# Kernel optimization log

Measured on AMD Instinct MI355X. Metric: run time of the kernel, lower is better.

## Reference

```python
import jax, jax.numpy as jnp
import numpy as np

B, T, C, NH = 2, 2048, 1024, 16
HD = C // NH  # 64


def _ln(x, g, b, eps=1e-5):
    m = x.mean(-1, keepdims=True)
    v = ((x - m) ** 2).mean(-1, keepdims=True)
    return (x - m) / jnp.sqrt(v + eps) * g + b


def _ff(x, w1, b1, w2, b2):
    # Linear -> exact (erf) GELU -> Linear; dropout=0 (identity)
    return jax.nn.gelu(x @ w1 + b1, approximate=False) @ w2 + b2


def setup_inputs() -> dict:
    key = jax.random.key(0)
    ks = jax.random.split(key, 16)
    s = 0.02
    f32 = jnp.float32
    return {
        "x": jax.random.normal(ks[0], (B, T, C), f32),
        # SelfAttn qkv projection (torch Linear stored transposed: (in, out))
        "w_attn": jax.random.normal(ks[1], (C, 3 * C), f32) * s,
        "b_attn": jnp.zeros((3 * C,), f32),
        # SelfAttn's internal FeedForward
        "wa1": jax.random.normal(ks[2], (C, 4 * C), f32) * s,
        "ba1": jnp.zeros((4 * C,), f32),
        "wa2": jax.random.normal(ks[3], (4 * C, C), f32) * s,
        "ba2": jnp.zeros((C,), f32),
        # Block ln1
        "g1": jnp.ones((C,), f32),
        "be1": jnp.zeros((C,), f32),
        # Block FeedForward
        "wf1": jax.random.normal(ks[4], (C, 4 * C), f32) * s,
        "bf1": jnp.zeros((4 * C,), f32),
        "wf2": jax.random.normal(ks[5], (4 * C, C), f32) * s,
        "bf2": jnp.zeros((C,), f32),
        # Block ln2
        "g2": jnp.ones((C,), f32),
        "be2": jnp.zeros((C,), f32),
    }


def reference(x, w_attn, b_attn, wa1, ba1, wa2, ba2, g1, be1,
              wf1, bf1, wf2, bf2, g2, be2):
    Bx, Tx, Cx = x.shape
    qkv = x @ w_attn + b_attn  # (B, T, 3C)
    # NOTE: original splits as K, Q, V (in that order)
    K, Q, V = jnp.split(qkv, 3, axis=-1)

    def heads(t):  # (B, T, C) -> (B, NH, T, HD)
        return t.reshape(Bx, Tx, NH, HD).transpose(0, 2, 1, 3)

    Q, K, V = heads(Q), heads(K), heads(V)
    att = jnp.einsum('bhqd,bhkd->bhqk', Q, K) / np.float32(np.sqrt(HD))
    mask = jnp.tril(jnp.ones((Tx, Tx), bool))  # causal
    att = jnp.where(mask, att, -jnp.inf)
    att = jax.nn.softmax(att, axis=-1)
    y = jnp.einsum('bhqk,bhkd->bhqd', att, V)
    y = y.transpose(0, 2, 1, 3).reshape(Bx, Tx, Cx)
    # SelfAttn applies its own FeedForward (no output projection)
    y = _ff(y, wa1, ba1, wa2, ba2)
    # Block: post-sublayer LayerNorm, additive residuals
    x = x + _ln(y, g1, be1)
    x = x + _ln(_ff(x, wf1, bf1, wf2, bf2), g2, be2)
    return x
```

## Files before the change

### kernel.cpp

```cpp
#include <hip/hip_runtime.h>
#include <hip/hip_bf16.h>
#include <math.h>

#define Bz 2
#define Tz 2048
#define Cz 1024
#define NHz 16
#define HDz 64
#define Mz (Bz*Tz)

typedef unsigned short u16;
typedef __attribute__((ext_vector_type(8))) short bf16x8;
typedef __attribute__((ext_vector_type(4))) float f32x4;

__device__ __forceinline__ float bf2f(u16 u){
  union { unsigned int i; float f; } v; v.i = ((unsigned int)u) << 16; return v.f;
}
__device__ __forceinline__ u16 f2bf(float f){
  union { float f; unsigned int i; } v; v.f = f;
  return (u16)((v.i + 0x7fffu + ((v.i >> 16) & 1u)) >> 16);
}
__device__ __forceinline__ unsigned pack_bf_trunc(float a, float b){
  union { float f; unsigned u; } ua, ub; ua.f = a; ub.f = b;
  return (ua.u >> 16) | (ub.u & 0xffff0000u);
}
__device__ __forceinline__ float gelu_fast(float x){
  float x3 = x * x * x;
  float z2 = 1.5957691216057308f * (x + 0.044715f * x3);
  float e  = __expf(z2);
  float t  = 1.f - 2.f / (e + 1.f);
  return 0.5f * x * (1.f + t);
}

__device__ __forceinline__ void glds16(const void* g, void* l){
  __builtin_amdgcn_global_load_lds(
      (const __attribute__((address_space(1))) void*)g,
      (__attribute__((address_space(3))) void*)l, 16, 0, 0);
}

__device__ __forceinline__ void pbar(){
  asm volatile("" ::: "memory");
  __builtin_amdgcn_s_barrier();
  asm volatile("" ::: "memory");
}
#define VMCNT(n) asm volatile("s_waitcnt vmcnt(" #n ")" ::: "memory")

__global__ __launch_bounds__(256) void prep_kernel(
    const float* __restrict__ xin, u16* __restrict__ xout,
    const float* __restrict__ s0, const float* __restrict__ s1,
    const float* __restrict__ s2, const float* __restrict__ s3,
    const float* __restrict__ s4,
    u16* __restrict__ d0, u16* __restrict__ d1, u16* __restrict__ d2,
    u16* __restrict__ d3, u16* __restrict__ d4){
  if (blockIdx.x < 4096) {
    int i = blockIdx.x * 256 + threadIdx.x;
    float4 v = ((const float4*)xin)[i];
    u16 t[4] = { f2bf(v.x), f2bf(v.y), f2bf(v.z), f2bf(v.w) };
    *(uint2*)&xout[(size_t)i * 4] = *(const uint2*)t;
    return;
  }
  __shared__ float tile[32][33];
  const int t = blockIdx.x - 4096;
  const float* src; u16* dst; int K, N, local;
  if (t < 3072)       { src = s0; dst = d0; K = 1024; N = 3072; local = t; }
  else if (t < 7168)  { src = s1; dst = d1; K = 1024; N = 4096; local = t - 3072; }
  else if (t < 11264) { src = s2; dst = d2; K = 4096; N = 1024; local = t - 7168; }
  else if (t < 15360) { src = s3; dst = d3; K = 1024; N = 4096; local = t - 11264; }
  else                { src = s4; dst = d4; K = 4096; N = 1024; local = t - 15360; }
  const int NT = N >> 5;
  const int kb = (local / NT) * 32, nb = (local % NT) * 32;
  const int tx = threadIdx.x & 31, ty = threadIdx.x >> 5;
  #pragma unroll
  for (int r = ty; r < 32; r += 8)
    tile[r][tx] = src[(size_t)(kb + r) * N + nb + tx];
  __syncthreads();
  #pragma unroll
  for (int r = ty; r < 32; r += 8)
    dst[(size_t)(nb + r) * K + kb + tx] = f2bf(tile[tx][r]);
}

template<int ACT, int KLEN>
__global__ __launch_bounds__(512, 2) void gemm256_kernel(const u16* __restrict__ A,
                                                         const u16* __restrict__ Bt,
                                                         const float* __restrict__ bias,
                                                         u16* __restrict__ ob,
                                                         int N, int lda){
  __shared__ __align__(16) u16 As[2][256 * 64];
  __shared__ __align__(16) u16 Bs[2][256 * 64];
  const int tid  = threadIdx.x;
  const int lane = tid & 63;
  const int wave = tid >> 6;
  const int cc = lane & 15, quad = lane >> 4;
  const int wm = (wave >> 2) * 128;
  const int wn = (wave & 3) * 64;

  int flat = blockIdx.x + gridDim.x * blockIdx.y;
  const int nwg = gridDim.x * gridDim.y;
  flat = (flat & 7) * (nwg >> 3) + (flat >> 3);
  const int m0 = (flat & 15) * 256;
  const int n0 = (flat >> 4) * 256;

  const u16* Ak  = A  + (size_t)blockIdx.z * KLEN;
  const u16* Btk = Bt + (size_t)blockIdx.z * KLEN;

  int srow[2], scol[2];
  #pragma unroll
  for (int rnd = 0; rnd < 2; ++rnd) {
    const int ci = tid + rnd * 512;
    const int r = ci >> 3, cg = ci & 7;
    srow[rnd] = r;
    scol[rnd] = (cg ^ (r & 7)) * 8;
  }
  int colsw[2];
  #pragma unroll
  for (int s = 0; s < 2; ++s)
    colsw[s] = (s * 32 + quad * 8) ^ ((cc & 7) << 3);

  const auto stA = [&](int t) {
    u16* dstb = As[t & 1];
    const u16* src = Ak + (size_t)m0 * lda + t * 64;
    #pragma unroll
    for (int h = 0; h < 2; ++h)
      #pragma unroll
      for (int rnd = 0; rnd < 2; ++rnd)
        glds16(src + (size_t)(h * 128 + srow[rnd]) * lda + scol[rnd],
               dstb + h * 8192 + (tid + rnd * 512) * 8);
  };
  const auto stB = [&](int t) {
    u16* dstb = Bs[t & 1];
    const u16* src = Btk + (size_t)n0 * lda + t * 64;
    #pragma unroll
    for (int h = 0; h < 2; ++h)
      #pragma unroll
      for (int rnd = 0; rnd < 2; ++rnd)
        glds16(src + (size_t)(h * 128 + srow[rnd]) * lda + scol[rnd],
               dstb + h * 8192 + (tid + rnd * 512) * 8);
  };

  bf16x8 af[4][2];
  bf16x8 bfr[2][2][2];
  f32x4 acc[2][2][4][2] = {};

  const auto rdA = [&](int qa, int bsel) {
    #pragma unroll
    for (int f = 0; f < 4; ++f)
      #pragma unroll
      for (int s = 0; s < 2; ++s)
        af[f][s] = *(const bf16x8*)&As[bsel][(wm + qa * 64 + f * 16 + cc) * 64 + colsw[s]];
  };
  const auto rdB = [&](int qb, int bsel) {
    #pragma unroll
    for (int f = 0; f < 2; ++f)
      #pragma unroll
      for (int s = 0; s < 2; ++s)
        bfr[qb][f][s] = *(const bf16x8*)&Bs[bsel][(wn + qb * 32 + f * 16 + cc) * 64 + colsw[s]];
  };
  const auto mf32 = [&](int qa) {
    __builtin_amdgcn_s_setprio(1);
    #pragma unroll
    for (int qb = 0; qb < 2; ++qb)
      #pragma unroll
      for (int s = 0; s < 2; ++s)
        #pragma unroll
        for (int am = 0; am < 4; ++am)
          #pragma unroll
          for (int bn = 0; bn < 2; ++bn)
            acc[qa][qb][am][bn] = __builtin_amdgcn_mfma_f32_16x16x32_bf16(
                af[am][s], bfr[qb][bn][s], acc[qa][qb][am][bn], 0, 0, 0);
    __builtin_amdgcn_s_setprio(0);
  };
  const auto mf32b = [&](int qa) {
    __builtin_amdgcn_s_setprio(1);
    #pragma unroll
    for (int qb = 1; qb >= 0; --qb)
      #pragma unroll
      for (int s = 0; s < 2; ++s)
        #pragma unroll
        for (int am = 0; am < 4; ++am)
          #pragma unroll
          for (int bn = 0; bn < 2; ++bn)
            acc[qa][qb][am][bn] = __builtin_amdgcn_mfma_f32_16x16x32_bf16(
                af[am][s], bfr[qb][bn][s], acc[qa][qb][am][bn], 0, 0, 0);
    __builtin_amdgcn_s_setprio(0);
  };

  stB(0); stA(0);
  stB(1);
  VMCNT(4);
  pbar();

  constexpr int nIter = KLEN >> 7;
  for (int i = 0; i < nIter; ++i) {
    const int t = 2 * i;
    const bool more = (i + 1 < nIter);
    rdA(0, 0); rdB(0, 0); rdB(1, 0); stA(t + 1);
    pbar(); mf32(0); pbar();
    rdA(1, 0); if (more) stB(t + 2);
    pbar(); mf32b(1);
    if (more) { VMCNT(4); } else { VMCNT(0); }
    pbar();
    rdA(0, 1); rdB(0, 1); rdB(1, 1); if (more) stA(t + 2);
    pbar(); mf32(0); pbar();
    rdA(1, 1); if (more) stB(t + 3);
    pbar(); mf32b(1);
    if (more) { VMCNT(4); }
    pbar();
  }

  u16* obz = ob + (size_t)blockIdx.z * ((size_t)Mz * N);
  const float* bp = (blockIdx.z == 0) ? bias : nullptr;
  const int rbase = quad * 4;
  #pragma unroll
  for (int qa = 0; qa < 2; ++qa)
    #pragma unroll
    for (int qb = 0; qb < 2; ++qb)
      #pragma unroll
      for (int bn = 0; bn < 2; ++bn) {
        const int col = n0 + wn + qb * 32 + bn * 16 + cc;
        const float bv = bp ? bp[col] : 0.f;
        #pragma unroll
        for (int am = 0; am < 4; ++am)
          #pragma unroll
          for (int r = 0; r < 4; ++r) {
            const int row = m0 + wm + qa * 64 + am * 16 + rbase + r;
            float v = acc[qa][qb][am][bn][r] + bv;
            if (ACT == 1) v = gelu_fast(v);
            obz[(size_t)row * N + col] = f2bf(v);
          }
      }
}

__global__ __launch_bounds__(256) void vtrans_kernel(const u16* __restrict__ qkv,
                                                     u16* __restrict__ Vtb){
  __shared__ u16 Vl[64 * 72];
  const int tid = threadIdx.x;
  const int t0 = blockIdx.x * 64, h = blockIdx.y, b = blockIdx.z;
  const int bh = b * NHz + h;
  #pragma unroll
  for (int it = 0; it < 2; it++) {
    int c = tid + it * 256;
    int row = c >> 3, g = c & 7;
    *(uint4*)&Vl[row * 72 + g * 8] =
        *(const uint4*)(qkv + (size_t)(b * Tz + t0 + row) * (3 * Cz) + 2 * Cz + h * 64 + g * 8);
  }
  __syncthreads();
  #pragma unroll
  for (int it = 0; it < 2; it++) {
    int c = tid + it * 256;
    int d = c >> 3, tg = c & 7;
    u16 tmp[8];
    #pragma unroll
    for (int e = 0; e < 8; e++) tmp[e] = Vl[(tg * 8 + e) * 72 + d];
    *(uint4*)&Vtb[((size_t)bh * 64 + d) * Tz + t0 + tg * 8] = *(const uint4*)tmp;
  }
}

__global__ __launch_bounds__(256) void attn_kernel(const u16* __restrict__ qkv,
                                                   const u16* __restrict__ Vtb,
                                                   u16* __restrict__ y){
  __shared__ __align__(16) u16 KV[2][2][64 * 64];
  __shared__ __align__(16) u16 Ps[64 * 72];
  const int tid = threadIdx.x;
  const int lane = tid & 63, wave = tid >> 6;
  const int cc = lane & 15, quad = lane >> 4;
  const int flat = blockIdx.x;
  const int xcd = flat & 7, slot = flat >> 3;
  const int bhg = xcd * 4 + (slot >> 4);
  const int qtp = slot & 15;
  const int h = bhg & 15, b = bhg >> 4;
  const int bh = b * NHz + h;
  const size_t rowb = (size_t)b * Tz;
  const int wq0 = wave * 16;

  int foff[4][2];
  const int sw0 = (quad ^ (cc & 7)) * 8;
  const int sw1 = ((4 + quad) ^ (cc & 7)) * 8;
  #pragma unroll
  for (int t = 0; t < 4; ++t) {
    foff[t][0] = (t * 16 + cc) * 64 + sw0;
    foff[t][1] = (t * 16 + cc) * 64 + sw1;
  }
  const int pswb = (wq0 + cc) * 72 + quad * 4;
  const int psr0 = (wq0 + cc) * 72 + quad * 8;
  const int psr1 = (wq0 + cc) * 72 + 32 + quad * 8;

  auto stage = [&](int i, int bsel) {
    const int k0s = i * 64;
    #pragma unroll
    for (int it = 0; it < 2; ++it) {
      int ci = tid + it * 256;
      int row = ci >> 3, g = ci & 7;
      int gs = g ^ (row & 7);
      glds16(qkv + (rowb + k0s + row) * (3 * Cz) + h * 64 + gs * 8, &KV[bsel][0][ci * 8]);
      glds16(Vtb + ((size_t)bh * 64 + row) * Tz + k0s + gs * 8,     &KV[bsel][1][ci * 8]);
    }
  };

  for (int ph = 0; ph < 2; ++ph) {
    const int qt = ph ? (31 - qtp) : qtp;
    const int q0t = qt * 64 + wq0;
    const int nkt = qt + 1;
    const int wqmax = q0t + 15;

    bf16x8 qf[2];
    #pragma unroll
    for (int s = 0; s < 2; ++s)
      qf[s] = *(const bf16x8*)(qkv + (rowb + q0t + cc) * (3 * Cz)
                               + Cz + h * 64 + s * 32 + quad * 8);
    f32x4 acc[4] = {};
    float lp = 0.f;

    if (ph) __syncthreads();
    stage(0, 0);

    for (int i = 0; i < nkt; ++i) {
      __syncthreads();
      if (i + 1 < nkt) stage(i + 1, (i + 1) & 1);
      const int sel = i & 1;
      const u16* Kl = KV[sel][0];
      const u16* Vl = KV[sel][1];
      const int k0 = i * 64;
      if (k0 > wqmax) continue;

      bf16x8 kf[4][2];
      #pragma unroll
      for (int kt = 0; kt < 4; ++kt) {
        kf[kt][0] = *(const bf16x8*)&Kl[foff[kt][0]];
        kf[kt][1] = *(const bf16x8*)&Kl[foff[kt][1]];
      }
      const int qbase = q0t;
      #pragma unroll
      for (int kt = 0; kt < 4; ++kt) {
        const int kbase = k0 + kt * 16;
        uint2 pk;
        if (kbase > qbase + 15) {
          pk.x = 0u; pk.y = 0u;
        } else {
          f32x4 st = __builtin_amdgcn_mfma_f32_16x16x32_bf16(
              kf[kt][0], qf[0], (f32x4){0.f, 0.f, 0.f, 0.f}, 0, 0, 0);
          st = __builtin_amdgcn_mfma_f32_16x16x32_bf16(kf[kt][1], qf[1], st, 0, 0, 0);
          if (kbase + 15 > qbase) {
            const int kq = kbase + quad * 4, ql = qbase + cc;
            st[0] = (kq     <= ql) ? st[0] : -1e30f;
            st[1] = (kq + 1 <= ql) ? st[1] : -1e30f;
            st[2] = (kq + 2 <= ql) ? st[2] : -1e30f;
            st[3] = (kq + 3 <= ql) ? st[3] : -1e30f;
          }
          float p0 = __expf(fmaf(st[0], 0.125f, -16.f));
          float p1 = __expf(fmaf(st[1], 0.125f, -16.f));
          float p2 = __expf(fmaf(st[2], 0.125f, -16.f));
          float p3 = __expf(fmaf(st[3], 0.125f, -16.f));
          lp += (p0 + p1) + (p2 + p3);
          pk.x = pack_bf_trunc(p0, p1);
          pk.y = pack_bf_trunc(p2, p3);
        }
        *(uint2*)&Ps[pswb + kt * 16] = pk;
      }
      bf16x8 pf0 = *(const bf16x8*)&Ps[psr0];
      bf16x8 pf1 = *(const bf16x8*)&Ps[psr1];
      #pragma unroll
      for (int jd = 0; jd < 4; ++jd) {
        bf16x8 vf0 = *(const bf16x8*)&Vl[foff[jd][0]];
        bf16x8 vf1 = *(const bf16x8*)&Vl[foff[jd][1]];
        acc[jd] = __builtin_amdgcn_mfma_f32_16x16x32_bf16(pf0, vf0, acc[jd], 0, 0, 0);
        acc[jd] = __builtin_amdgcn_mfma_f32_16x16x32_bf16(pf1, vf1, acc[jd], 0, 0, 0);
      }
    }

    lp += __shfl_xor(lp, 16, 64);
    lp += __shfl_xor(lp, 32, 64);
    float inv[4];
    #pragma unroll
    for (int r = 0; r < 4; ++r) inv[r] = 1.f / __shfl(lp, quad * 4 + r, 64);
    #pragma unroll
    for (int jd = 0; jd < 4; ++jd)
      #pragma unroll
      for (int r = 0; r < 4; ++r) {
        int qrow = q0t + quad * 4 + r;
        y[(rowb + qrow) * Cz + h * 64 + jd * 16 + cc] = f2bf(acc[jd][r] * inv[r]);
      }
  }
}

__global__ __launch_bounds__(256) void ln_resid_kernel(const float* __restrict__ xf,
                                                       const u16* __restrict__ xb16,
                                                       const u16* __restrict__ yp,
                                                       const float* __restrict__ g,
                                                       const float* __restrict__ be,
                                                       float* __restrict__ outf,
                                                       u16* __restrict__ outb){
  const int row = blockIdx.x;
  const int c0 = threadIdx.x * 4;
  const size_t base = (size_t)row * Cz + c0;
  float4 v; v.x = 0.f; v.y = 0.f; v.z = 0.f; v.w = 0.f;
  #pragma unroll
  for (int p = 0; p < 4; ++p) {
    uint2 pp = *(const uint2*)(yp + (size_t)p * ((size_t)Mz * Cz) + base);
    v.x += bf2f((u16)(pp.x & 0xffff)); v.y += bf2f((u16)(pp.x >> 16));
    v.z += bf2f((u16)(pp.y & 0xffff)); v.w += bf2f((u16)(pp.y >> 16));
  }
  float s  = v.x + v.y + v.z + v.w;
  float s2 = v.x*v.x + v.y*v.y + v.z*v.z + v.w*v.w;
  #pragma unroll
  for (int off = 32; off > 0; off >>= 1) {
    s  += __shfl_down(s,  off);
    s2 += __shfl_down(s2, off);
  }
  __shared__ float ps[4], ps2[4];
  int wave = threadIdx.x >> 6, lane = threadIdx.x & 63;
  if (lane == 0) { ps[wave] = s; ps2[wave] = s2; }
  __syncthreads();
  s  = ps[0]  + ps[1]  + ps[2]  + ps[3];
  s2 = ps2[0] + ps2[1] + ps2[2] + ps2[3];
  const float mean = s * (1.f / Cz);
  const float var  = s2 * (1.f / Cz) - mean * mean;
  const float rstd = rsqrtf(var + 1e-5f);
  float4 xv;
  if (xf) {
    xv = *(const float4*)(xf + base);
  } else {
    uint2 px = *(const uint2*)(xb16 + base);
    xv.x = bf2f((u16)(px.x & 0xffff)); xv.y = bf2f((u16)(px.x >> 16));
    xv.z = bf2f((u16)(px.y & 0xffff)); xv.w = bf2f((u16)(px.y >> 16));
  }
  float4 gv = *(const float4*)(g + c0);
  float4 bv = *(const float4*)(be + c0);
  float4 ov;
  ov.x = xv.x + (v.x - mean) * rstd * gv.x + bv.x;
  ov.y = xv.y + (v.y - mean) * rstd * gv.y + bv.y;
  ov.z = xv.z + (v.z - mean) * rstd * gv.z + bv.z;
  ov.w = xv.w + (v.w - mean) * rstd * gv.w + bv.w;
  if (outf) *(float4*)(outf + base) = ov;
  if (outb) {
    u16 t[4] = { f2bf(ov.x), f2bf(ov.y), f2bf(ov.z), f2bf(ov.w) };
    *(ulonglong1*)&outb[base] = *(const ulonglong1*)t;
  }
}

extern "C" void kernel_launch(void* const* d_in, const int* in_sizes, int n_in,
                              void* d_out, int out_size, void* d_ws, size_t ws_size,
                              hipStream_t stream) {
  const float* x      = (const float*)d_in[0];
  const float* w_attn = (const float*)d_in[1];
  const float* b_attn = (const float*)d_in[2];
  const float* wa1    = (const float*)d_in[3];
  const float* ba1    = (const float*)d_in[4];
  const float* wa2    = (const float*)d_in[5];
  const float* ba2    = (const float*)d_in[6];
  const float* g1     = (const float*)d_in[7];
  const float* be1    = (const float*)d_in[8];
  const float* wf1    = (const float*)d_in[9];
  const float* bf1    = (const float*)d_in[10];
  const float* wf2    = (const float*)d_in[11];
  const float* bf2    = (const float*)d_in[12];
  const float* g2     = (const float*)d_in[13];
  const float* be2    = (const float*)d_in[14];
  float* out = (float*)d_out;

  char* ws = (char*)d_ws;
  size_t off = 0;
  auto alloc = [&](size_t bytes) { size_t o = off; off += (bytes + 255) & ~(size_t)255; return o; };
  u16* qkvb    = (u16*)(ws + alloc((size_t)Mz * 3 * Cz * 2));
  u16* ybuf    = (u16*)(ws + alloc((size_t)Mz * Cz * 2));
  u16* xb      = (u16*)(ws + alloc((size_t)Mz * Cz * 2));
  u16* wT_attn = (u16*)(ws + alloc((size_t)3 * Cz * Cz * 2));
  u16* wT_a1   = (u16*)(ws + alloc((size_t)4 * Cz * Cz * 2));
  u16* Vtb     = (u16*)(ws + alloc((size_t)Bz * NHz * HDz * Tz * 2));
  u16* wT_a2   = (u16*)(ws + alloc((size_t)4 * Cz * Cz * 2));
  u16* wT_f1   = (u16*)(ws + alloc((size_t)4 * Cz * Cz * 2));
  u16* wT_f2   = (u16*)(ws + alloc((size_t)4 * Cz * Cz * 2));
  u16* hbuf    = (u16*)(ws + alloc((size_t)Mz * 4 * Cz * 2));
  u16* pb      = (u16*)(ws + alloc((size_t)4 * Mz * Cz * 2));
  u16* x1b     = (u16*)(ws + alloc((size_t)Mz * Cz * 2));
  alloc(256);
  (void)ws_size; (void)in_sizes; (void)n_in; (void)out_size;

  prep_kernel<<<4096 + 19456, 256, 0, stream>>>(x, xb, w_attn, wa1, wa2, wf1, wf2,
                                                wT_attn, wT_a1, wT_a2, wT_f1, wT_f2);

  gemm256_kernel<0, Cz><<<dim3(16, 12, 1), 512, 0, stream>>>(xb, wT_attn, b_attn,
      qkvb, 3*Cz, Cz);

  vtrans_kernel<<<dim3(Tz/64, NHz, Bz), 256, 0, stream>>>(qkvb, Vtb);
  attn_kernel<<<dim3(512, 1, 1), 256, 0, stream>>>(qkvb, Vtb, ybuf);

  gemm256_kernel<1, Cz><<<dim3(16, 16, 1), 512, 0, stream>>>(ybuf, wT_a1, ba1,
      hbuf, 4*Cz, Cz);
  gemm256_kernel<0, Cz><<<dim3(16, 4, 4), 512, 0, stream>>>(hbuf, wT_a2, ba2,
      pb, Cz, 4*Cz);

  ln_resid_kernel<<<Mz, 256, 0, stream>>>(x, nullptr, pb, g1, be1,
                                          nullptr, x1b);

  gemm256_kernel<1, Cz><<<dim3(16, 16, 1), 512, 0, stream>>>(x1b, wT_f1, bf1,
      hbuf, 4*Cz, Cz);
  gemm256_kernel<0, Cz><<<dim3(16, 4, 4), 512, 0, stream>>>(hbuf, wT_f2, bf2,
      pb, Cz, 4*Cz);

  ln_resid_kernel<<<Mz, 256, 0, stream>>>(nullptr, x1b, pb, g2, be2,
                                          out, nullptr);
}
```

Measured before the change: 443.7 us.

## Replace 256x256 GEMM tiles with simpler 128x128 tiles and single-stage loop

Swaps the 256x256x64 eight-wave GEMM, which had a hand-interleaved ping-pong schedule, for a 128x128x32 four-wave kernel. The new kernel prefetches the next K-slice into a double buffer, then waits on all loads and barriers every iteration. Grids grow fourfold to give more workgroups and higher occupancy (launch bounds 256,4). The cost is lower per-tile data reuse and loss of the fine-grained overlap and priority tricks of the old schedule.

```diff
diff --git a/kernel.cpp b/kernel.cpp
--- a/kernel.cpp
+++ b/kernel.cpp
@@ -79,131 +79,75 @@
     dst[(size_t)(nb + r) * K + kb + tx] = f2bf(tile[tx][r]);
 }
 
-template<int ACT, int KLEN>
-__global__ __launch_bounds__(512, 2) void gemm256_kernel(const u16* __restrict__ A,
+template<int ACT>
+__global__ __launch_bounds__(256, 4) void gemm128_kernel(const u16* __restrict__ A,
                                                          const u16* __restrict__ Bt,
                                                          const float* __restrict__ bias,
                                                          u16* __restrict__ ob,
                                                          int N, int lda){
-  __shared__ __align__(16) u16 As[2][256 * 64];
-  __shared__ __align__(16) u16 Bs[2][256 * 64];
+  __shared__ __align__(16) u16 As[2][128 * 32];
+  __shared__ __align__(16) u16 Bs[2][128 * 32];
   const int tid  = threadIdx.x;
   const int lane = tid & 63;
   const int wave = tid >> 6;
   const int cc = lane & 15, quad = lane >> 4;
-  const int wm = (wave >> 2) * 128;
-  const int wn = (wave & 3) * 64;
+  const int wm = (wave >> 1) * 64;
+  const int wn = (wave & 1) * 64;
 
   int flat = blockIdx.x + gridDim.x * blockIdx.y;
   const int nwg = gridDim.x * gridDim.y;
   flat = (flat & 7) * (nwg >> 3) + (flat >> 3);
-  const int m0 = (flat & 15) * 256;
-  const int n0 = (flat >> 4) * 256;
-
-  const u16* Ak  = A  + (size_t)blockIdx.z * KLEN;
-  const u16* Btk = Bt + (size_t)blockIdx.z * KLEN;
+  const int m0 = (flat & 31) * 128;
+  const int n0 = (flat >> 5) * 128;
+
+  const u16* Ak  = A  + (size_t)blockIdx.z * 1024;
+  const u16* Btk = Bt + (size_t)blockIdx.z * 1024;
 
   int srow[2], scol[2];
   #pragma unroll
   for (int rnd = 0; rnd < 2; ++rnd) {
-    const int ci = tid + rnd * 512;
-    const int r = ci >> 3, cg = ci & 7;
+    const int ci = tid + rnd * 256;
+    const int r = ci >> 2, cg = ci & 3;
     srow[rnd] = r;
-    scol[rnd] = (cg ^ (r & 7)) * 8;
-  }
-  int colsw[2];
-  #pragma unroll
-  for (int s = 0; s < 2; ++s)
-    colsw[s] = (s * 32 + quad * 8) ^ ((cc & 7) << 3);
-
-  const auto stA = [&](int t) {
-    u16* dstb = As[t & 1];
-    const u16* src = Ak + (size_t)m0 * lda + t * 64;
-    #pragma unroll
-    for (int h = 0; h < 2; ++h)
-      #pragma unroll
-      for (int rnd = 0; rnd < 2; ++rnd)
-        glds16(src + (size_t)(h * 128 + srow[rnd]) * lda + scol[rnd],
-               dstb + h * 8192 + (tid + rnd * 512) * 8);
+    scol[rnd] = (cg ^ (r & 3)) * 8;
+  }
+  const int colsw = (quad ^ (cc & 3)) * 8;
+
+  const auto stage = [&](int t, int bsel) {
+    u16* da = As[bsel];
+    u16* db = Bs[bsel];
+    const u16* sa = Ak  + (size_t)m0 * lda + t * 32;
+    const u16* sb = Btk + (size_t)n0 * lda + t * 32;
+    #pragma unroll
+    for (int rnd = 0; rnd < 2; ++rnd) {
+      glds16(sa + (size_t)srow[rnd] * lda + scol[rnd], da + (tid + rnd * 256) * 8);
+      glds16(sb + (size_t)srow[rnd] * lda + scol[rnd], db + (tid + rnd * 256) * 8);
+    }
   };
-  const auto stB = [&](int t) {
-    u16* dstb = Bs[t & 1];
-    const u16* src = Btk + (size_t)n0 * lda + t * 64;
-    #pragma unroll
-    for (int h = 0; h < 2; ++h)
-      #pragma unroll
-      for (int rnd = 0; rnd < 2; ++rnd)
-        glds16(src + (size_t)(h * 128 + srow[rnd]) * lda + scol[rnd],
-               dstb + h * 8192 + (tid + rnd * 512) * 8);
-  };
-
-  bf16x8 af[4][2];
-  bf16x8 bfr[2][2][2];
-  f32x4 acc[2][2][4][2] = {};
-
-  const auto rdA = [&](int qa, int bsel) {
+
+  f32x4 acc[4][4] = {};
+
+  const int nt = 32;
+  stage(0, 0);
+  VMCNT(0);
+  pbar();
+
+  for (int t = 0; t < nt; ++t) {
+    const int sel = t & 1;
+    if (t + 1 < nt) stage(t + 1, sel ^ 1);
+    bf16x8 af[4], bfr[4];
     #pragma unroll
     for (int f = 0; f < 4; ++f)
-      #pragma unroll
-      for (int s = 0; s < 2; ++s)
-        af[f][s] = *(const bf16x8*)&As[bsel][(wm + qa * 64 + f * 16 + cc) * 64 + colsw[s]];
-  };
-  const auto rdB = [&](int qb, int bsel) {
-    #pragma unroll
-    for (int f = 0; f < 2; ++f)
-      #pragma unroll
-      for (int s = 0; s < 2; ++s)
-        bfr[qb][f][s] = *(const bf16x8*)&Bs[bsel][(wn + qb * 32 + f * 16 + cc) * 64 + colsw[s]];
-  };
-  const auto mf32 = [&](int qa) {
-    __builtin_amdgcn_s_setprio(1);
-    #pragma unroll
-    for (int qb = 0; qb < 2; ++qb)
-      #pragma unroll
-      for (int s = 0; s < 2; ++s)
-        #pragma unroll
-        for (int am = 0; am < 4; ++am)
-          #pragma unroll
-          for (int bn = 0; bn < 2; ++bn)
-            acc[qa][qb][am][bn] = __builtin_amdgcn_mfma_f32_16x16x32_bf16(
-                af[am][s], bfr[qb][bn][s], acc[qa][qb][am][bn], 0, 0, 0);
-    __builtin_amdgcn_s_setprio(0);
-  };
-  const auto mf32b = [&](int qa) {
-    __builtin_amdgcn_s_setprio(1);
-    #pragma unroll
-    for (int qb = 1; qb >= 0; --qb)
-      #pragma unroll
-      for (int s = 0; s < 2; ++s)
-        #pragma unroll
-        for (int am = 0; am < 4; ++am)
-          #pragma unroll
-          for (int bn = 0; bn < 2; ++bn)
-            acc[qa][qb][am][bn] = __builtin_amdgcn_mfma_f32_16x16x32_bf16(
-                af[am][s], bfr[qb][bn][s], acc[qa][qb][am][bn], 0, 0, 0);
-    __builtin_amdgcn_s_setprio(0);
-  };
-
-  stB(0); stA(0);
-  stB(1);
-  VMCNT(4);
-  pbar();
-
-  constexpr int nIter = KLEN >> 7;
-  for (int i = 0; i < nIter; ++i) {
-    const int t = 2 * i;
-    const bool more = (i + 1 < nIter);
-    rdA(0, 0); rdB(0, 0); rdB(1, 0); stA(t + 1);
-    pbar(); mf32(0); pbar();
-    rdA(1, 0); if (more) stB(t + 2);
-    pbar(); mf32b(1);
-    if (more) { VMCNT(4); } else { VMCNT(0); }
-    pbar();
-    rdA(0, 1); rdB(0, 1); rdB(1, 1); if (more) stA(t + 2);
-    pbar(); mf32(0); pbar();
-    rdA(1, 1); if (more) stB(t + 3);
-    pbar(); mf32b(1);
-    if (more) { VMCNT(4); }
+      af[f]  = *(const bf16x8*)&As[sel][(wm + f * 16 + cc) * 32 + colsw];
+    #pragma unroll
+    for (int f = 0; f < 4; ++f)
+      bfr[f] = *(const bf16x8*)&Bs[sel][(wn + f * 16 + cc) * 32 + colsw];
+    #pragma unroll
+    for (int i = 0; i < 4; ++i)
+      #pragma unroll
+      for (int j = 0; j < 4; ++j)
+        acc[i][j] = __builtin_amdgcn_mfma_f32_16x16x32_bf16(af[i], bfr[j], acc[i][j], 0, 0, 0);
+    VMCNT(0);
     pbar();
   }
 
@@ -211,23 +155,19 @@
   const float* bp = (blockIdx.z == 0) ? bias : nullptr;
   const int rbase = quad * 4;
   #pragma unroll
-  for (int qa = 0; qa < 2; ++qa)
-    #pragma unroll
-    for (int qb = 0; qb < 2; ++qb)
-      #pragma unroll
-      for (int bn = 0; bn < 2; ++bn) {
-        const int col = n0 + wn + qb * 32 + bn * 16 + cc;
-        const float bv = bp ? bp[col] : 0.f;
-        #pragma unroll
-        for (int am = 0; am < 4; ++am)
-          #pragma unroll
-          for (int r = 0; r < 4; ++r) {
-            const int row = m0 + wm + qa * 64 + am * 16 + rbase + r;
-            float v = acc[qa][qb][am][bn][r] + bv;
-            if (ACT == 1) v = gelu_fast(v);
-            obz[(size_t)row * N + col] = f2bf(v);
-          }
+  for (int i = 0; i < 4; ++i)
+    #pragma unroll
+    for (int j = 0; j < 4; ++j) {
+      const int col = n0 + wn + j * 16 + cc;
+      const float bv = bp ? bp[col] : 0.f;
+      #pragma unroll
+      for (int r = 0; r < 4; ++r) {
+        const int row = m0 + wm + i * 16 + rbase + r;
+        float v = acc[i][j][r] + bv;
+        if (ACT == 1) v = gelu_fast(v);
+        obz[(size_t)row * N + col] = f2bf(v);
       }
+    }
 }
 
 __global__ __launch_bounds__(256) void vtrans_kernel(const u16* __restrict__ qkv,
@@ -478,23 +418,23 @@
   prep_kernel<<<4096 + 19456, 256, 0, stream>>>(x, xb, w_attn, wa1, wa2, wf1, wf2,
                                                 wT_attn, wT_a1, wT_a2, wT_f1, wT_f2);
 
-  gemm256_kernel<0, Cz><<<dim3(16, 12, 1), 512, 0, stream>>>(xb, wT_attn, b_attn,
+  gemm128_kernel<0><<<dim3(32, 24, 1), 256, 0, stream>>>(xb, wT_attn, b_attn,
       qkvb, 3*Cz, Cz);
 
   vtrans_kernel<<<dim3(Tz/64, NHz, Bz), 256, 0, stream>>>(qkvb, Vtb);
   attn_kernel<<<dim3(512, 1, 1), 256, 0, stream>>>(qkvb, Vtb, ybuf);
 
-  gemm256_kernel<1, Cz><<<dim3(16, 16, 1), 512, 0, stream>>>(ybuf, wT_a1, ba1,
+  gemm128_kernel<1><<<dim3(32, 32, 1), 256, 0, stream>>>(ybuf, wT_a1, ba1,
       hbuf, 4*Cz, Cz);
-  gemm256_kernel<0, Cz><<<dim3(16, 4, 4), 512, 0, stream>>>(hbuf, wT_a2, ba2,
+  gemm128_kernel<0><<<dim3(32, 8, 4), 256, 0, stream>>>(hbuf, wT_a2, ba2,
       pb, Cz, 4*Cz);
 
   ln_resid_kernel<<<Mz, 256, 0, stream>>>(x, nullptr, pb, g1, be1,
                                           nullptr, x1b);
 
-  gemm256_kernel<1, Cz><<<dim3(16, 16, 1), 512, 0, stream>>>(x1b, wT_f1, bf1,
+  gemm128_kernel<1><<<dim3(32, 32, 1), 256, 0, stream>>>(x1b, wT_f1, bf1,
       hbuf, 4*Cz, Cz);
-  gemm256_kernel<0, Cz><<<dim3(16, 4, 4), 512, 0, stream>>>(hbuf, wT_f2, bf2,
+  gemm128_kernel<0><<<dim3(32, 8, 4), 256, 0, stream>>>(hbuf, wT_f2, bf2,
       pb, Cz, 4*Cz);
 
   ln_resid_kernel<<<Mz, 256, 0, stream>>>(nullptr, x1b, pb, g2, be2,
```

New measurement: 484.3 us. 1.09x slower.

## Use 128x128 tiles with 2-way split-K for the down-projection GEMMs

Applied to the files above, without the earlier changes.

Adds a 128x128-tile, 256-thread GEMM kernel with swizzled LDS and an XCD-aware block remap, and uses it for the two 4C->C projections with 2-way split-K instead of a 256-tile kernel with 4-way split-K. Fewer K splits halve the bf16 partial-sum buffer traffic written by the GEMM and read back in the LayerNorm kernel, and the smaller tiles give 512 workgroups to occupy the CUs. The new kernel is single-buffered, with two barriers per K step and no load/compute overlap, so per-tile efficiency may fall below the larger kernel's.

```diff
diff --git a/kernel.cpp b/kernel.cpp
--- a/kernel.cpp
+++ b/kernel.cpp
@@ -228,6 +228,96 @@
             obz[(size_t)row * N + col] = f2bf(v);
           }
       }
+}
+
+template<int ACT, int KLEN>
+__global__ __launch_bounds__(256, 3) void gemm128s_kernel(const u16* __restrict__ A,
+                                                          const u16* __restrict__ Bt,
+                                                          const float* __restrict__ bias,
+                                                          u16* __restrict__ ob,
+                                                          int N, int lda){
+  __shared__ __align__(16) u16 As[128 * 64];
+  __shared__ __align__(16) u16 Bs[128 * 64];
+  const int tid  = threadIdx.x;
+  const int lane = tid & 63;
+  const int wave = tid >> 6;
+  const int cc = lane & 15, quad = lane >> 4;
+  const int wm = (wave >> 1) * 64;
+  const int wn = (wave & 1) * 64;
+
+  int flat = blockIdx.x + gridDim.x * blockIdx.y;
+  const int nwg = gridDim.x * gridDim.y;
+  flat = (flat & 7) * (nwg >> 3) + (flat >> 3);
+  const int m0 = (flat & 31) * 128;
+  const int n0 = (flat >> 5) * 128;
+
+  const u16* Ak  = A  + (size_t)blockIdx.z * KLEN;
+  const u16* Btk = Bt + (size_t)blockIdx.z * KLEN;
+
+  int srow[4], scol[4];
+  #pragma unroll
+  for (int rnd = 0; rnd < 4; ++rnd) {
+    const int ci = tid + rnd * 256;
+    const int r = ci >> 3, cg = ci & 7;
+    srow[rnd] = r;
+    scol[rnd] = (cg ^ (r & 7)) * 8;
+  }
+  int colsw[2];
+  #pragma unroll
+  for (int s = 0; s < 2; ++s)
+    colsw[s] = (s * 32 + quad * 8) ^ ((cc & 7) << 3);
+
+  const auto stage = [&](int t) {
+    const u16* sa = Ak  + (size_t)m0 * lda + t * 64;
+    const u16* sb = Btk + (size_t)n0 * lda + t * 64;
+    #pragma unroll
+    for (int rnd = 0; rnd < 4; ++rnd) {
+      glds16(sa + (size_t)srow[rnd] * lda + scol[rnd], As + (tid + rnd * 256) * 8);
+      glds16(sb + (size_t)srow[rnd] * lda + scol[rnd], Bs + (tid + rnd * 256) * 8);
+    }
+  };
+
+  f32x4 acc[4][4] = {};
+
+  constexpr int nt = KLEN >> 6;
+  for (int t = 0; t < nt; ++t) {
+    __syncthreads();
+    stage(t);
+    __syncthreads();
+    #pragma unroll
+    for (int s = 0; s < 2; ++s) {
+      bf16x8 af[4], bfr[4];
+      #pragma unroll
+      for (int f = 0; f < 4; ++f)
+        af[f]  = *(const bf16x8*)&As[(wm + f * 16 + cc) * 64 + colsw[s]];
+      #pragma unroll
+      for (int f = 0; f < 4; ++f)
+        bfr[f] = *(const bf16x8*)&Bs[(wn + f * 16 + cc) * 64 + colsw[s]];
+      #pragma unroll
+      for (int i = 0; i < 4; ++i)
+        #pragma unroll
+        for (int j = 0; j < 4; ++j)
+          acc[i][j] = __builtin_amdgcn_mfma_f32_16x16x32_bf16(af[i], bfr[j], acc[i][j], 0, 0, 0);
+    }
+  }
+
+  u16* obz = ob + (size_t)blockIdx.z * ((size_t)Mz * N);
+  const float* bp = (blockIdx.z == 0) ? bias : nullptr;
+  const int rbase = quad * 4;
+  #pragma unroll
+  for (int i = 0; i < 4; ++i)
+    #pragma unroll
+    for (int j = 0; j < 4; ++j) {
+      const int col = n0 + wn + j * 16 + cc;
+      const float bv = bp ? bp[col] : 0.f;
+      #pragma unroll
+      for (int r = 0; r < 4; ++r) {
+        const int row = m0 + wm + i * 16 + rbase + r;
+        float v = acc[i][j][r] + bv;
+        if (ACT == 1) v = gelu_fast(v);
+        obz[(size_t)row * N + col] = f2bf(v);
+      }
+    }
 }
 
 __global__ __launch_bounds__(256) void vtrans_kernel(const u16* __restrict__ qkv,
@@ -394,7 +484,7 @@
   const size_t base = (size_t)row * Cz + c0;
   float4 v; v.x = 0.f; v.y = 0.f; v.z = 0.f; v.w = 0.f;
   #pragma unroll
-  for (int p = 0; p < 4; ++p) {
+  for (int p = 0; p < 2; ++p) {
     uint2 pp = *(const uint2*)(yp + (size_t)p * ((size_t)Mz * Cz) + base);
     v.x += bf2f((u16)(pp.x & 0xffff)); v.y += bf2f((u16)(pp.x >> 16));
     v.z += bf2f((u16)(pp.y & 0xffff)); v.w += bf2f((u16)(pp.y >> 16));
@@ -470,7 +560,7 @@
   u16* wT_f1   = (u16*)(ws + alloc((size_t)4 * Cz * Cz * 2));
   u16* wT_f2   = (u16*)(ws + alloc((size_t)4 * Cz * Cz * 2));
   u16* hbuf    = (u16*)(ws + alloc((size_t)Mz * 4 * Cz * 2));
-  u16* pb      = (u16*)(ws + alloc((size_t)4 * Mz * Cz * 2));
+  u16* pb      = (u16*)(ws + alloc((size_t)2 * Mz * Cz * 2));
   u16* x1b     = (u16*)(ws + alloc((size_t)Mz * Cz * 2));
   alloc(256);
   (void)ws_size; (void)in_sizes; (void)n_in; (void)out_size;
@@ -486,7 +576,7 @@
 
   gemm256_kernel<1, Cz><<<dim3(16, 16, 1), 512, 0, stream>>>(ybuf, wT_a1, ba1,
       hbuf, 4*Cz, Cz);
-  gemm256_kernel<0, Cz><<<dim3(16, 4, 4), 512, 0, stream>>>(hbuf, wT_a2, ba2,
+  gemm128s_kernel<0, 2048><<<dim3(32, 8, 2), 256, 0, stream>>>(hbuf, wT_a2, ba2,
       pb, Cz, 4*Cz);
 
   ln_resid_kernel<<<Mz, 256, 0, stream>>>(x, nullptr, pb, g1, be1,
@@ -494,7 +584,7 @@
 
   gemm256_kernel<1, Cz><<<dim3(16, 16, 1), 512, 0, stream>>>(x1b, wT_f1, bf1,
       hbuf, 4*Cz, Cz);
-  gemm256_kernel<0, Cz><<<dim3(16, 4, 4), 512, 0, stream>>>(hbuf, wT_f2, bf2,
+  gemm128s_kernel<0, 2048><<<dim3(32, 8, 2), 256, 0, stream>>>(hbuf, wT_f2, bf2,
       pb, Cz, 4*Cz);
 
   ln_resid_kernel<<<Mz, 256, 0, stream>>>(nullptr, x1b, pb, g2, be2,
```

Measured after the change: 445.0 us. No clear change (+0.3%).
